# Optimization experiments

Measured on AMD Instinct MI355X. Metric: run time of the kernel, lower is better.

Reference implementation:

```python
import jax, jax.numpy as jnp
import numpy as np
import math

B, L, D, H = 2, 2048, 1024, 16
d = D // H

def setup_inputs() -> dict:
    key = jax.random.key(0)
    ks = jax.random.split(key, 12)
    s = 0.02
    return {
        "x": jax.random.normal(ks[0], (B, L, D), jnp.float32),
        "Wqkv_w": jax.random.normal(ks[1], (D, 3 * D), jnp.float32) * s,
        "Wqkv_b": jax.random.normal(ks[2], (3 * D,), jnp.float32) * s,
        "out_w": jax.random.normal(ks[3], (D, D), jnp.float32) * s,
        "out_b": jax.random.normal(ks[4], (D,), jnp.float32) * s,
        "W_static": jnp.zeros((H, d, d), jnp.float32),
        "Lambda_raw": jax.random.uniform(ks[5], (H, d, d), jnp.float32, -3.0, 3.0),
        "Gamma": jax.random.uniform(ks[6], (H, d, d), jnp.float32, -0.5 / math.sqrt(d), 0.5 / math.sqrt(d)),
        "gate_w1": jax.random.normal(ks[7], (D, D // 2), jnp.float32) * s,
        "gate_b1": jax.random.normal(ks[8], (D // 2,), jnp.float32) * s,
        "gate_w2": jax.random.normal(ks[9], (D // 2, H), jnp.float32) * s,
        "gate_b2": jax.random.normal(ks[10], (H,), jnp.float32) * s,
    }

def _forward(x, Wqkv_w, Wqkv_b, out_w, out_b, W_static, Lambda_raw, Gamma,
             gate_w1, gate_b1, gate_w2, gate_b2):
    scale = 1.0 / math.sqrt(d)
    qkv = x @ Wqkv_w + Wqkv_b                              # (B,L,3D)
    qkv = qkv.reshape(B, L, 3, H, d).transpose(2, 0, 3, 1, 4)  # (3,B,H,L,d)
    q, k, v = qkv[0], qkv[1], qkv[2]

    # --- causal softmax attention branch ---
    scores = jnp.einsum('bhid,bhjd->bhij', q, k) * scale
    mask = jnp.triu(jnp.full((L, L), -10000.0, scores.dtype), 1)
    attn = jax.nn.softmax(scores + mask, axis=-1)
    y_softmax = jnp.einsum('bhij,bhjd->bhid', attn, v)     # (B,H,L,d)

    # --- STP fast-weight branch: decaying Hebbian state recurrence ---
    k_stp = k * scale
    retention = 1.0 - jax.nn.sigmoid(Lambda_raw)           # (H,d,d)
    def step(state, qkv_t):
        q_t, k_t, v_t = qkv_t                              # each (B,H,d)
        hebbian = v_t[..., :, None] * k_t[..., None, :]    # (B,H,d,d)
        state = retention * state + Gamma * hebbian
        y_t = jnp.einsum('bhij,bhj->bhi', W_static + state, q_t)
        return state, y_t
    qkv_seq = (q.transpose(2, 0, 1, 3), k_stp.transpose(2, 0, 1, 3), v.transpose(2, 0, 1, 3))
    state0 = jnp.zeros((B, H, d, d), x.dtype)
    _, y_stp = jax.lax.scan(step, state0, qkv_seq)         # (L,B,H,d)
    y_stp = y_stp.transpose(1, 2, 0, 3)                    # (B,H,L,d)

    # --- learned gate ---
    h = jax.nn.gelu(x @ gate_w1 + gate_b1, approximate=False)
    alpha = jax.nn.sigmoid(h @ gate_w2 + gate_b2)          # (B,L,H)
    alpha = alpha.transpose(0, 2, 1)[..., None]            # (B,H,L,1)

    y = alpha * y_softmax + (1.0 - alpha) * y_stp          # (B,H,L,d)
    y = y.transpose(0, 2, 1, 3).reshape(B, L, D)
    return y @ out_w + out_b

def reference(x, Wqkv_w, Wqkv_b, out_w, out_b, W_static, Lambda_raw, Gamma,
              gate_w1, gate_b1, gate_w2, gate_b2):
    return _forward(x, Wqkv_w, Wqkv_b, out_w, out_b, W_static, Lambda_raw, Gamma,
                    gate_w1, gate_b1, gate_w2, gate_b2)
```

## Files before the change

### kernel.cpp

```cpp
#include <hip/hip_runtime.h>
#include <cstdint>
#include <cstddef>

#define B_ 2
#define L_ 2048
#define D_ 1024
#define H_ 16
#define DH 64

typedef __attribute__((ext_vector_type(8))) short bf16x8;
typedef __attribute__((ext_vector_type(4))) float f32x4;
typedef unsigned short u16;

__device__ inline u16 f2bf(float f) {
  unsigned u = __builtin_bit_cast(unsigned, f);
  u += 0x7fffu + ((u >> 16) & 1u);
  return (u16)(u >> 16);
}

__device__ inline float bf2f(u16 x) {
  return __builtin_bit_cast(float, (unsigned)x << 16);
}

template <int CTRL>
__device__ inline float dpp_mov(float x) {
  int t = __builtin_amdgcn_update_dpp(0, __builtin_bit_cast(int, x), CTRL, 0xf, 0xf, true);
  return __builtin_bit_cast(float, t);
}

#define GLDS16(ldst, gsrc)                                              \
  __builtin_amdgcn_global_load_lds(                                    \
      (const __attribute__((address_space(1))) void*)(gsrc),           \
      (__attribute__((address_space(3))) void*)(ldst), 16, 0, 0)

__device__ inline void stp_upd(float4& z, const float4 r, const float4 g,
                               const float4 wlc, float vv,
                               float kx, float ky, float kz, float kw) {
  z.x = fmaf(r.x, z.x, fmaf(g.x * vv, kx, wlc.x));
  z.y = fmaf(r.y, z.y, fmaf(g.y * vv, ky, wlc.y));
  z.z = fmaf(r.z, z.z, fmaf(g.z * vv, kz, wlc.z));
  z.w = fmaf(r.w, z.w, fmaf(g.w * vv, kw, wlc.w));
}

__device__ inline void stp_upd1(float4& z, const float4 r, const float4 g,
                                float vv, float kx, float ky, float kz, float kw) {
  z.x = fmaf(r.x, z.x, (g.x * vv) * kx);
  z.y = fmaf(r.y, z.y, (g.y * vv) * ky);
  z.z = fmaf(r.z, z.z, (g.z * vv) * kz);
  z.w = fmaf(r.w, z.w, (g.w * vv) * kw);
}

__device__ inline float stp_dot(const float4 z, float qx, float qy, float qz, float qw) {
  float p = z.x * qx;
  p = fmaf(z.y, qy, p);
  p = fmaf(z.z, qz, p);
  p = fmaf(z.w, qw, p);
  return p;
}

__device__ inline float dpp_red16(float p) {
  p = p + dpp_mov<0x128>(p);
  p = p + dpp_mov<0x124>(p);
  p = p + dpp_mov<0x122>(p);
  p = p + dpp_mov<0x121>(p);
  return p;
}


__device__ inline void d_transpose(const float* __restrict__ in,
                                   u16* __restrict__ out, int R, int C,
                                   int bx, int by, float tile[32][33], int tid) {
  const int tx = tid & 31, ty = tid >> 5;
  const int c0 = bx * 32, r0 = by * 32;
#pragma unroll
  for (int j = 0; j < 4; ++j)
    tile[ty + j * 8][tx] = in[(size_t)(r0 + ty + j * 8) * C + c0 + tx];
  __syncthreads();
#pragma unroll
  for (int j = 0; j < 4; ++j)
    out[(size_t)(c0 + ty + j * 8) * R + r0 + tx] = f2bf(tile[tx][ty + j * 8]);
}

__global__ __launch_bounds__(256) void prep_fused(
    const float* __restrict__ x, u16* __restrict__ xbf,
    const float* __restrict__ wqkv_w, u16* __restrict__ wqkvT,
    const float* __restrict__ out_w, u16* __restrict__ owT,
    const float* __restrict__ g_w1, u16* __restrict__ g1T,
    const float* __restrict__ lam, const float* __restrict__ gma,
    float* __restrict__ retb, float* __restrict__ gamb,
    float* __restrict__ retb64) {
  __shared__ float tile[32][33];
  const int bid = blockIdx.x, tid = threadIdx.x;
  if (bid < 4096) {
    int i = bid * 256 + tid;
    float4 v = ((const float4*)x)[i];
    ushort4 o;
    o.x = f2bf(v.x); o.y = f2bf(v.y); o.z = f2bf(v.z); o.w = f2bf(v.w);
    ((ushort4*)xbf)[i] = o;
  } else if (bid < 7168) {
    int r = bid - 4096;
    d_transpose(wqkv_w, wqkvT, 1024, 3072, r % 96, r / 96, tile, tid);
  } else if (bid < 8192) {
    int r = bid - 7168;
    d_transpose(out_w, owT, 1024, 1024, r % 32, r / 32, tile, tid);
  } else if (bid < 8704) {
    int r = bid - 8192;
    d_transpose(g_w1, g1T, 1024, 512, r % 16, r / 16, tile, tid);
  } else {
    int i = (bid - 8704) * 256 + tid;
    float l = lam[i];
    float r = 1.f / (1.f + expf(l));
    retb[i] = r;
    gamb[i] = gma[i] * 0.125f;
    float r2 = r * r;
    float r4 = r2 * r2;
    float r8 = r4 * r4;
    float r16 = r8 * r8;
    float r32 = r16 * r16;
    retb64[i] = r32 * r32;
  }
}


struct GemmP {
  const u16* A; const u16* Bt; int M, N, K;
  const float* bias;
  u16* qb; u16* kb; u16* vtb;
  float* hout;
  float* outp;
};

template <int EPI>
__device__ void gemm_body(const GemmP& p, int lin0, int nwgx, int nwgtot,
                          u16* As, u16* Bs, u16* tileT) {
  const int tid = threadIdx.x;
  const int lane = tid & 63;
  const int w = tid >> 6;
  const int wr = w >> 1, wc = w & 1;
  const int lr = lane & 15, lk = lane >> 4;
  const int cpx = nwgtot >> 3;
  const int lin = (lin0 & 7) * cpx + (lin0 >> 3);
  const int m0 = (lin / nwgx) * 128, n0 = (lin % nwgx) * 128;

  f32x4 acc[4][4];
#pragma unroll
  for (int i = 0; i < 4; ++i)
#pragma unroll
    for (int j = 0; j < 4; ++j) acc[i][j] = (f32x4){0.f, 0.f, 0.f, 0.f};

  for (int k0 = 0; k0 < p.K; k0 += 32) {
    __syncthreads();
#pragma unroll
    for (int it = 0; it < 2; ++it) {
      int idx = it * 256 + tid;
      int row = idx >> 2, ch = idx & 3;
      GLDS16(&As[idx * 8], p.A + (size_t)(m0 + row) * p.K + k0 + ch * 8);
      GLDS16(&Bs[idx * 8], p.Bt + (size_t)(n0 + row) * p.K + k0 + ch * 8);
    }
    __syncthreads();
    bf16x8 af[4], bfr[4];
#pragma unroll
    for (int mr = 0; mr < 4; ++mr)
      af[mr] = *(const bf16x8*)&As[(wr * 64 + mr * 16 + lr) * 32 + lk * 8];
#pragma unroll
    for (int nr = 0; nr < 4; ++nr)
      bfr[nr] = *(const bf16x8*)&Bs[(wc * 64 + nr * 16 + lr) * 32 + lk * 8];
#pragma unroll
    for (int mr = 0; mr < 4; ++mr)
#pragma unroll
      for (int nr = 0; nr < 4; ++nr)
        acc[mr][nr] = __builtin_amdgcn_mfma_f32_16x16x32_bf16(af[mr], bfr[nr], acc[mr][nr], 0, 0, 0);
  }

  if constexpr (EPI == 0) {
    if (n0 < 2048) {
#pragma unroll
      for (int mr = 0; mr < 4; ++mr)
#pragma unroll
        for (int nr = 0; nr < 4; ++nr) {
          const int col = n0 + wc * 64 + nr * 16 + lr;
#pragma unroll
          for (int rr = 0; rr < 4; ++rr) {
            const int row = m0 + wr * 64 + mr * 16 + lk * 4 + rr;
            float v = acc[mr][nr][rr] + p.bias[col];
            int which = col >> 10, hh = (col >> 6) & 15, ii = col & 63;
            int b = row >> 11, ll = row & 2047;
            size_t bi = ((size_t)(b * 16 + hh) * L_ + ll) * 64 + ii;
            if (which == 0) p.qb[bi] = f2bf(v * 0.125f);
            else            p.kb[bi] = f2bf(v);
          }
        }
    } else {
#pragma unroll
      for (int mr = 0; mr < 4; ++mr)
#pragma unroll
        for (int nr = 0; nr < 4; ++nr) {
          const int cl = wc * 64 + nr * 16 + lr;
          const float bv = p.bias[n0 + cl];
#pragma unroll
          for (int rr = 0; rr < 4; ++rr) {
            const int rl = wr * 64 + mr * 16 + lk * 4 + rr;
            tileT[cl * 136 + rl] = f2bf(acc[mr][nr][rr] + bv);
          }
        }
      __syncthreads();
      const int c = tid >> 1, h = tid & 1;
      const int vcol = (n0 - 2048) + c;
      const int hh = vcol >> 6, ii = vcol & 63;
      const int b = m0 >> 11;
      const int ll0 = (m0 & 2047) + h * 64;
      u16* dst = p.vtb + ((size_t)(b * 16 + hh) * 64 + ii) * L_ + ll0;
      const u16* src = &tileT[c * 136 + h * 64];
#pragma unroll
      for (int k = 0; k < 8; ++k)
        *(int4*)(dst + k * 8) = *(const int4*)(src + k * 8);
    }
  } else {
#pragma unroll
    for (int mr = 0; mr < 4; ++mr)
#pragma unroll
      for (int nr = 0; nr < 4; ++nr) {
        const int col = n0 + wc * 64 + nr * 16 + lr;
#pragma unroll
        for (int rr = 0; rr < 4; ++rr) {
          const int row = m0 + wr * 64 + mr * 16 + lk * 4 + rr;
          float v = acc[mr][nr][rr] + p.bias[col];
          if constexpr (EPI == 1) {
            float g = 0.5f * v * (1.f + erff(v * 0.70710678118f));
            p.hout[(size_t)row * p.N + col] = g;
          } else {
            p.outp[(size_t)row * p.N + col] = v;
          }
        }
      }
  }
}

__global__ __launch_bounds__(256, 2) void gemm01_kernel(GemmP p0, GemmP p1) {
  __shared__ u16 As[128 * 32];
  __shared__ u16 Bs[128 * 32];
  __shared__ u16 tileT[128 * 136];
  const int bid = blockIdx.x;
  if (bid < 768) gemm_body<0>(p0, bid, 24, 768, As, Bs, tileT);
  else           gemm_body<1>(p1, bid - 768, 4, 128, As, Bs, tileT);
}

__global__ __launch_bounds__(256, 2) void gemm2_kernel(GemmP p) {
  __shared__ u16 As[128 * 32];
  __shared__ u16 Bs[128 * 32];
  const int lin0 = (int)blockIdx.x + 8 * (int)blockIdx.y;
  gemm_body<2>(p, lin0, 8, 256, As, Bs, nullptr);
}


__global__ __launch_bounds__(256) void alpha_kernel(
    const float* __restrict__ hbuf, const float* __restrict__ w2,
    const float* __restrict__ b2, float* __restrict__ alp) {
  const int tid = threadIdx.x;
  const int row = blockIdx.x * 16 + (tid >> 4);
  const int n = tid & 15;
  const float4* h4 = (const float4*)(hbuf + (size_t)row * 512);
  float acc = 0.f;
#pragma unroll 2
  for (int kk = 0; kk < 128; ++kk) {
    float4 hv = h4[kk];
    acc = fmaf(hv.x, w2[(kk * 4 + 0) * 16 + n], acc);
    acc = fmaf(hv.y, w2[(kk * 4 + 1) * 16 + n], acc);
    acc = fmaf(hv.z, w2[(kk * 4 + 2) * 16 + n], acc);
    acc = fmaf(hv.w, w2[(kk * 4 + 3) * 16 + n], acc);
  }
  float z = acc + b2[n];
  alp[row * 16 + n] = 1.f / (1.f + __expf(-z));
}


__device__ void attn_body(int lin, u16* sbuf,
                          const u16* __restrict__ qb, const u16* __restrict__ kb,
                          const u16* __restrict__ vtb, float* __restrict__ ysm) {
  u16* Ks = sbuf;
  u16* Vts = sbuf + 4096;
  u16* Pl = sbuf + 8192;
  const int tid = threadIdx.x, lane = tid & 63, w = tid >> 6;
  const int lr = lane & 15, lk = lane >> 4;
  const int bh = lin & 31;
  const int xp = lin >> 5;
  const int qtA = 31 - xp, qtB = xp;

  const u16* kbase0 = kb + (size_t)bh * (L_ * 64);
  const u16* vbase0 = vtb + (size_t)bh * (64 * L_);

  const size_t qbaseA = ((size_t)bh * L_ + qtA * 64 + w * 16 + lr) * 64;
  const size_t qbaseB = ((size_t)bh * L_ + qtB * 64 + w * 16 + lr) * 64;
  bf16x8 qfrA[2], qfrB[2];
  qfrA[0] = *(const bf16x8*)(qb + qbaseA + lk * 8);
  qfrA[1] = *(const bf16x8*)(qb + qbaseA + 32 + lk * 8);
  qfrB[0] = *(const bf16x8*)(qb + qbaseB + lk * 8);
  qfrB[1] = *(const bf16x8*)(qb + qbaseB + 32 + lk * 8);

  f32x4 yaccA[4], yaccB[4];
  float mrowA[4], lrowA[4], mrowB[4], lrowB[4];
#pragma unroll
  for (int i = 0; i < 4; ++i) {
    yaccA[i] = (f32x4){0.f, 0.f, 0.f, 0.f};
    yaccB[i] = (f32x4){0.f, 0.f, 0.f, 0.f};
    mrowA[i] = -1e30f; mrowB[i] = -1e30f;
    lrowA[i] = 0.f;    lrowB[i] = 0.f;
  }

  auto process = [&](const bf16x8* qfr, f32x4* yacc, float* mrow, float* lrow,
                     bool maskTile) {
    f32x4 s[4];
#pragma unroll
    for (int f = 0; f < 4; ++f) {
      f32x4 sf = (f32x4){0.f, 0.f, 0.f, 0.f};
#pragma unroll
      for (int ss = 0; ss < 2; ++ss) {
        bf16x8 kfr = *(const bf16x8*)&Ks[(f * 16 + lr) * 64 +
                                         (((ss * 4 + lk) ^ (lr & 7)) * 8)];
        sf = __builtin_amdgcn_mfma_f32_16x16x32_bf16(qfr[ss], kfr, sf, 0, 0, 0);
      }
      s[f] = sf;
    }
    if (maskTile) {
#pragma unroll
      for (int f = 0; f < 4; ++f)
#pragma unroll
        for (int rr = 0; rr < 4; ++rr)
          if (f * 16 + lr > w * 16 + lk * 4 + rr) s[f][rr] = -1e30f;
    }
    float mx[4];
#pragma unroll
    for (int rr = 0; rr < 4; ++rr) {
      float m = fmaxf(fmaxf(s[0][rr], s[1][rr]), fmaxf(s[2][rr], s[3][rr]));
      m = fmaxf(m, dpp_mov<0x128>(m));
      m = fmaxf(m, dpp_mov<0x124>(m));
      m = fmaxf(m, dpp_mov<0x122>(m));
      m = fmaxf(m, dpp_mov<0x121>(m));
      mx[rr] = m;
    }
    bool need = (mx[0] > mrow[0] + 8.f) | (mx[1] > mrow[1] + 8.f) |
                (mx[2] > mrow[2] + 8.f) | (mx[3] > mrow[3] + 8.f);
    if (__any(need)) {
#pragma unroll
      for (int rr = 0; rr < 4; ++rr) {
        float mn = fmaxf(mrow[rr], mx[rr]);
        float c = __expf(mrow[rr] - mn);
        lrow[rr] *= c;
#pragma unroll
        for (int nf = 0; nf < 4; ++nf) yacc[nf][rr] *= c;
        mrow[rr] = mn;
      }
    }
    u16* pw = Pl + w * 1024;
#pragma unroll
    for (int rr = 0; rr < 4; ++rr) {
      const int prow = lk * 4 + rr;
      float rs = 0.f;
#pragma unroll
      for (int f = 0; f < 4; ++f) {
        float pv = __expf(s[f][rr] - mrow[rr]);
        rs += pv;
        int chunk = f * 2 + (lr >> 3);
        pw[prow * 64 + ((chunk ^ (prow & 7)) * 8) + (lr & 7)] = f2bf(pv);
      }
      rs = rs + dpp_mov<0x128>(rs);
      rs = rs + dpp_mov<0x124>(rs);
      rs = rs + dpp_mov<0x122>(rs);
      rs = rs + dpp_mov<0x121>(rs);
      lrow[rr] += rs;
    }
#pragma unroll
    for (int s2 = 0; s2 < 2; ++s2) {
      bf16x8 pa = *(const bf16x8*)&pw[lr * 64 + (((s2 * 4 + lk) ^ (lr & 7)) * 8)];
#pragma unroll
      for (int nf = 0; nf < 4; ++nf) {
        bf16x8 vfr = *(const bf16x8*)&Vts[(nf * 16 + lr) * 64 +
                                          (((s2 * 4 + lk) ^ (lr & 7)) * 8)];
        yacc[nf] = __builtin_amdgcn_mfma_f32_16x16x32_bf16(pa, vfr, yacc[nf], 0, 0, 0);
      }
    }
  };

  const int nkv = qtA + 1;
  for (int kt = 0; kt < nkv; ++kt) {
    const int kv0 = kt * 64;
    __syncthreads();
#pragma unroll
    for (int it = 0; it < 2; ++it) {
      int idx = it * 256 + tid;
      int row = idx >> 3, ch = idx & 7;
      int sch = (ch ^ (row & 7)) * 8;
      *(int4*)&Ks[row * 64 + sch] =
          *(const int4*)(kbase0 + (size_t)(kv0 + row) * 64 + ch * 8);
      *(int4*)&Vts[row * 64 + sch] =
          *(const int4*)(vbase0 + (size_t)row * L_ + kv0 + ch * 8);
    }
    __syncthreads();

    process(qfrA, yaccA, mrowA, lrowA, kt == qtA);
    if (kt <= qtB) process(qfrB, yaccB, mrowB, lrowB, kt == qtB);
  }

#pragma unroll
  for (int nf = 0; nf < 4; ++nf)
#pragma unroll
    for (int rr = 0; rr < 4; ++rr) {
      int rowl = w * 16 + lk * 4 + rr;
      int col = nf * 16 + lr;
      ysm[((size_t)bh * L_ + qtA * 64 + rowl) * 64 + col] = yaccA[nf][rr] / lrowA[rr];
      ysm[((size_t)bh * L_ + qtB * 64 + rowl) * 64 + col] = yaccB[nf][rr] / lrowB[rr];
    }
}


__device__ void stp1_body(int bid, u16* Klds,
                          const u16* __restrict__ kb, const u16* __restrict__ vtb,
                          const float* __restrict__ retb,
                          const float* __restrict__ gamb,
                          float* __restrict__ slocal) {
  const int tid = threadIdx.x, lane = tid & 63, w = tid >> 6;
  const int bh = bid >> 5, c = bid & 31;
  const int hh = bh & 15;
  const int m = lane >> 4, j4 = (lane & 15) * 4;
  const int i0m = w * 16 + m * 4;

  const u16* kcb = kb + ((size_t)bh * L_ + c * 64) * 64;
  GLDS16(&Klds[tid * 8], kcb + tid * 8);
  GLDS16(&Klds[2048 + tid * 8], kcb + 2048 + tid * 8);
  __syncthreads();

  const int hij = (hh * 64 + i0m) * 64 + j4;
  const float4 r0 = *(const float4*)(retb + hij);
  const float4 r1 = *(const float4*)(retb + hij + 64);
  const float4 r2 = *(const float4*)(retb + hij + 128);
  const float4 r3 = *(const float4*)(retb + hij + 192);
  const float4 g0 = *(const float4*)(gamb + hij);
  const float4 g1 = *(const float4*)(gamb + hij + 64);
  const float4 g2 = *(const float4*)(gamb + hij + 128);
  const float4 g3 = *(const float4*)(gamb + hij + 192);
  const u16* vbp = vtb + ((size_t)bh * 64 + i0m) * L_ + c * 64;

  float4 s0 = {0,0,0,0}, s1 = {0,0,0,0}, s2 = {0,0,0,0}, s3 = {0,0,0,0};
#pragma unroll 1
  for (int t8 = 0; t8 < 8; ++t8) {
    const bf16x8 va = *(const bf16x8*)(vbp + t8 * 8);
    const bf16x8 vb = *(const bf16x8*)(vbp + L_ + t8 * 8);
    const bf16x8 vc = *(const bf16x8*)(vbp + 2 * L_ + t8 * 8);
    const bf16x8 vd = *(const bf16x8*)(vbp + 3 * L_ + t8 * 8);
#pragma unroll
    for (int tt = 0; tt < 8; ++tt) {
      const ushort4 k4u = *(const ushort4*)&Klds[(t8 * 8 + tt) * 64 + j4];
      const float kx = bf2f(k4u.x), ky = bf2f(k4u.y),
                  kz = bf2f(k4u.z), kw = bf2f(k4u.w);
      stp_upd1(s0, r0, g0, bf2f((u16)va[tt]), kx, ky, kz, kw);
      stp_upd1(s1, r1, g1, bf2f((u16)vb[tt]), kx, ky, kz, kw);
      stp_upd1(s2, r2, g2, bf2f((u16)vc[tt]), kx, ky, kz, kw);
      stp_upd1(s3, r3, g3, bf2f((u16)vd[tt]), kx, ky, kz, kw);
    }
  }
  float* sb = slocal + (((size_t)(bh * 32 + c) * 64) + i0m) * 64 + j4;
  *(float4*)(sb)       = s0;
  *(float4*)(sb + 64)  = s1;
  *(float4*)(sb + 128) = s2;
  *(float4*)(sb + 192) = s3;
}

__global__ __launch_bounds__(256, 2) void attn_stp1_kernel(
    const u16* __restrict__ qb, const u16* __restrict__ kb,
    const u16* __restrict__ vtb, float* __restrict__ ysm,
    const float* __restrict__ retb, const float* __restrict__ gamb,
    float* __restrict__ slocal) {
  __shared__ u16 sbuf[12288];
  const int bid = blockIdx.x;
  if (bid < 512) attn_body(bid, sbuf, qb, kb, vtb, ysm);
  else           stp1_body(bid - 512, sbuf, kb, vtb, retb, gamb, slocal);
}

__global__ __launch_bounds__(256) void stp_scan(
    const float* __restrict__ retb64, float* __restrict__ slocal) {
  const int idx = blockIdx.x * 256 + threadIdx.x;
  const int j = idx & 63, i1 = (idx >> 6) & 63, bh = idx >> 12;
  const int hh = bh & 15;
  const float r64 = retb64[(hh * 64 + i1) * 64 + j];
  float carry = 0.f;
  for (int c = 0; c < 32; ++c) {
    const size_t off = ((((size_t)bh * 32 + c) * 64 + i1) * 64 + j);
    const float sl = slocal[off];
    slocal[off] = carry;
    carry = fmaf(r64, carry, sl);
  }
}

__global__ __launch_bounds__(256, 4) void stp_pass2(
    const u16* __restrict__ qb, const u16* __restrict__ kb,
    const u16* __restrict__ vtb, const float* __restrict__ retb,
    const float* __restrict__ gamb, const float* __restrict__ wst,
    const float* __restrict__ slocal, float* __restrict__ ystp) {
  __shared__ u16 KQ[8192];
  const int tid = threadIdx.x, lane = tid & 63, w = tid >> 6;
  const int bh = blockIdx.x >> 5, c = blockIdx.x & 31;
  const int hh = bh & 15;
  const int m = lane >> 4, jc = lane & 15, j4 = jc * 4;
  const int i0m = w * 16 + m * 4;

  const size_t cb = ((size_t)bh * L_ + c * 64) * 64;
  GLDS16(&KQ[tid * 8], kb + cb + tid * 8);
  GLDS16(&KQ[2048 + tid * 8], kb + cb + 2048 + tid * 8);
  GLDS16(&KQ[4096 + tid * 8], qb + cb + tid * 8);
  GLDS16(&KQ[6144 + tid * 8], qb + cb + 2048 + tid * 8);
  __syncthreads();

  const int hij = (hh * 64 + i0m) * 64 + j4;
  const float4 r0 = *(const float4*)(retb + hij);
  const float4 r1 = *(const float4*)(retb + hij + 64);
  const float4 r2 = *(const float4*)(retb + hij + 128);
  const float4 r3 = *(const float4*)(retb + hij + 192);
  const float4 g0 = *(const float4*)(gamb + hij);
  const float4 g1 = *(const float4*)(gamb + hij + 64);
  const float4 g2 = *(const float4*)(gamb + hij + 128);
  const float4 g3 = *(const float4*)(gamb + hij + 192);
  const float4 w0 = *(const float4*)(wst + hij);
  const float4 w1 = *(const float4*)(wst + hij + 64);
  const float4 w2 = *(const float4*)(wst + hij + 128);
  const float4 w3 = *(const float4*)(wst + hij + 192);

  const float* sb = slocal + (((size_t)(bh * 32 + c) * 64) + i0m) * 64 + j4;
  float4 z0 = *(const float4*)(sb);
  float4 z1 = *(const float4*)(sb + 64);
  float4 z2 = *(const float4*)(sb + 128);
  float4 z3 = *(const float4*)(sb + 192);

  float4 wlc0, wlc1, wlc2, wlc3;
  wlc0.x = w0.x * (1.f - r0.x); wlc0.y = w0.y * (1.f - r0.y);
  wlc0.z = w0.z * (1.f - r0.z); wlc0.w = w0.w * (1.f - r0.w);
  wlc1.x = w1.x * (1.f - r1.x); wlc1.y = w1.y * (1.f - r1.y);
  wlc1.z = w1.z * (1.f - r1.z); wlc1.w = w1.w * (1.f - r1.w);
  wlc2.x = w2.x * (1.f - r2.x); wlc2.y = w2.y * (1.f - r2.y);
  wlc2.z = w2.z * (1.f - r2.z); wlc2.w = w2.w * (1.f - r2.w);
  wlc3.x = w3.x * (1.f - r3.x); wlc3.y = w3.y * (1.f - r3.y);
  wlc3.z = w3.z * (1.f - r3.z); wlc3.w = w3.w * (1.f - r3.w);
  z0.x += w0.x; z0.y += w0.y; z0.z += w0.z; z0.w += w0.w;
  z1.x += w1.x; z1.y += w1.y; z1.z += w1.z; z1.w += w1.w;
  z2.x += w2.x; z2.y += w2.y; z2.z += w2.z; z2.w += w2.w;
  z3.x += w3.x; z3.y += w3.y; z3.z += w3.z; z3.w += w3.w;

  const u16* vbp = vtb + ((size_t)bh * 64 + i0m) * L_ + c * 64;
  float* yp = ystp + cb + i0m;

#pragma unroll 1
  for (int t8 = 0; t8 < 8; ++t8) {
    const bf16x8 va = *(const bf16x8*)(vbp + t8 * 8);
    const bf16x8 vb = *(const bf16x8*)(vbp + L_ + t8 * 8);
    const bf16x8 vc = *(const bf16x8*)(vbp + 2 * L_ + t8 * 8);
    const bf16x8 vd = *(const bf16x8*)(vbp + 3 * L_ + t8 * 8);
#pragma unroll
    for (int tt = 0; tt < 8; ++tt) {
      const int t = t8 * 8 + tt;
      const ushort4 k4u = *(const ushort4*)&KQ[t * 64 + j4];
      const ushort4 q4u = *(const ushort4*)&KQ[4096 + t * 64 + j4];
      const float kx = bf2f(k4u.x), ky = bf2f(k4u.y),
                  kz = bf2f(k4u.z), kw = bf2f(k4u.w);
      const float qx = bf2f(q4u.x), qy = bf2f(q4u.y),
                  qz = bf2f(q4u.z), qw = bf2f(q4u.w);
      stp_upd(z0, r0, g0, wlc0, bf2f((u16)va[tt]), kx, ky, kz, kw);
      stp_upd(z1, r1, g1, wlc1, bf2f((u16)vb[tt]), kx, ky, kz, kw);
      stp_upd(z2, r2, g2, wlc2, bf2f((u16)vc[tt]), kx, ky, kz, kw);
      stp_upd(z3, r3, g3, wlc3, bf2f((u16)vd[tt]), kx, ky, kz, kw);
      float p0 = dpp_red16(stp_dot(z0, qx, qy, qz, qw));
      float p1 = dpp_red16(stp_dot(z1, qx, qy, qz, qw));
      float p2 = dpp_red16(stp_dot(z2, qx, qy, qz, qw));
      float p3 = dpp_red16(stp_dot(z3, qx, qy, qz, qw));
      if (jc == 0) {
        float4 yo;
        yo.x = p0 * 8.f; yo.y = p1 * 8.f; yo.z = p2 * 8.f; yo.w = p3 * 8.f;
        *(float4*)(yp + t * 64) = yo;
      }
    }
  }
}


__global__ __launch_bounds__(256) void blend_kernel(
    const float* __restrict__ ysm, const float* __restrict__ ystp,
    const float* __restrict__ alp, u16* __restrict__ ycomb) {
  int idx = blockIdx.x * 256 + threadIdx.x;
  int m = idx >> 8;
  int n4 = (idx & 255) * 4;
  int hh = n4 >> 6, ii = n4 & 63;
  int b = m >> 11, ll = m & 2047;
  size_t bi = ((size_t)(b * 16 + hh) * L_ + ll) * 64 + ii;
  float a = alp[m * 16 + hh];
  float4 s = *(const float4*)(ysm + bi);
  float4 t = *(const float4*)(ystp + bi);
  ushort4 o;
  o.x = f2bf(a * s.x + (1.f - a) * t.x);
  o.y = f2bf(a * s.y + (1.f - a) * t.y);
  o.z = f2bf(a * s.z + (1.f - a) * t.z);
  o.w = f2bf(a * s.w + (1.f - a) * t.w);
  *(ushort4*)(ycomb + (size_t)m * 1024 + n4) = o;
}


extern "C" void kernel_launch(void* const* d_in, const int* in_sizes, int n_in,
                              void* d_out, int out_size, void* d_ws, size_t ws_size,
                              hipStream_t stream) {
  const float* x       = (const float*)d_in[0];
  const float* wqkv_w  = (const float*)d_in[1];
  const float* wqkv_b  = (const float*)d_in[2];
  const float* out_w   = (const float*)d_in[3];
  const float* out_b   = (const float*)d_in[4];
  const float* w_stat  = (const float*)d_in[5];
  const float* lam     = (const float*)d_in[6];
  const float* gma     = (const float*)d_in[7];
  const float* g_w1    = (const float*)d_in[8];
  const float* g_b1    = (const float*)d_in[9];
  const float* g_w2    = (const float*)d_in[10];
  const float* g_b2    = (const float*)d_in[11];

  char* ws = (char*)d_ws;
  size_t off = 0;
  auto nxt = [&](size_t b) { size_t r = off; off += (b + 255) & ~(size_t)255; return r; };
  u16*   xbf   = (u16*)(ws + nxt((size_t)4096 * 1024 * 2));
  u16*   wqkvT = (u16*)(ws + nxt((size_t)3072 * 1024 * 2));
  u16*   owT   = (u16*)(ws + nxt((size_t)1024 * 1024 * 2));
  u16*   g1T   = (u16*)(ws + nxt((size_t)512 * 1024 * 2));
  u16*   qb    = (u16*)(ws + nxt((size_t)4194304 * 2));
  u16*   kb    = (u16*)(ws + nxt((size_t)4194304 * 2));
  u16*   vtb   = (u16*)(ws + nxt((size_t)4194304 * 2));
  float* ysm   = (float*)(ws + nxt((size_t)4194304 * 4));
  float* ystp  = (float*)(ws + nxt((size_t)4194304 * 4));
  size_t hbuf_off = nxt((size_t)4096 * 512 * 4);
  float* hbuf  = (float*)(ws + hbuf_off);
  u16*   ycomb = (u16*)(ws + nxt((size_t)4096 * 1024 * 2));
  float* slocal = (float*)(ws + hbuf_off);
  float* alp   = (float*)(ws + nxt((size_t)4096 * 16 * 4));
  float* retb  = (float*)(ws + nxt((size_t)65536 * 4));
  float* gamb  = (float*)(ws + nxt((size_t)65536 * 4));
  float* retb64= (float*)(ws + nxt((size_t)65536 * 4));

  dim3 blk(256);
  prep_fused<<<8960, blk, 0, stream>>>(x, xbf, wqkv_w, wqkvT, out_w, owT,
                                       g_w1, g1T, lam, gma, retb, gamb, retb64);

  GemmP p0 = {xbf, wqkvT, 4096, 3072, 1024, wqkv_b,
              qb, kb, vtb, nullptr, nullptr};
  GemmP p1 = {xbf, g1T, 4096, 512, 1024, g_b1,
              nullptr, nullptr, nullptr, hbuf, nullptr};
  gemm01_kernel<<<896, blk, 0, stream>>>(p0, p1);

  alpha_kernel<<<256, blk, 0, stream>>>(hbuf, g_w2, g_b2, alp);

  attn_stp1_kernel<<<1536, blk, 0, stream>>>(qb, kb, vtb, ysm,
                                             retb, gamb, slocal);

  stp_scan<<<512, blk, 0, stream>>>(retb64, slocal);
  stp_pass2<<<1024, blk, 0, stream>>>(qb, kb, vtb, retb, gamb, w_stat,
                                      slocal, ystp);

  blend_kernel<<<4096, blk, 0, stream>>>(ysm, ystp, alp, ycomb);

  GemmP p2 = {ycomb, owT, 4096, 1024, 1024, out_b,
              nullptr, nullptr, nullptr, nullptr, (float*)d_out};
  gemm2_kernel<<<dim3(8, 32), blk, 0, stream>>>(p2);
}
```

Measured before the change: 252.8 us.

## Split fused attention/STP kernel; run paired query tiles on separate wave groups

The fused attention plus STP pass-1 kernel is split into two separate launches. Attention now uses 512-thread blocks in which two groups of four waves each handle one of the paired query tiles (one long, one short) at the same time instead of one after the other, sharing the K/V tiles staged in LDS. This raises per-block parallelism and lowers register pressure per wave. In exchange, the attention and STP work can no longer overlap within a single launch, there is an extra kernel launch, and the waves handling the shorter tile sit idle at barriers once their tile is done.

```diff
diff --git a/kernel.cpp b/kernel.cpp
--- a/kernel.cpp
+++ b/kernel.cpp
@@ -274,41 +274,40 @@
 }
 
 
-__device__ void attn_body(int lin, u16* sbuf,
-                          const u16* __restrict__ qb, const u16* __restrict__ kb,
-                          const u16* __restrict__ vtb, float* __restrict__ ysm) {
-  u16* Ks = sbuf;
-  u16* Vts = sbuf + 4096;
-  u16* Pl = sbuf + 8192;
+__global__ __launch_bounds__(512, 4) void attn_kernel(
+    const u16* __restrict__ qb, const u16* __restrict__ kb,
+    const u16* __restrict__ vtb, float* __restrict__ ysm) {
+  __shared__ u16 Ks[64 * 64];
+  __shared__ u16 Vts[64 * 64];
+  __shared__ u16 Pl[8][1024];
   const int tid = threadIdx.x, lane = tid & 63, w = tid >> 6;
+  const int wg = w >> 2;
+  const int wl = w & 3;
   const int lr = lane & 15, lk = lane >> 4;
+  const int lin = (int)blockIdx.x + 16 * (int)blockIdx.y;
   const int bh = lin & 31;
   const int xp = lin >> 5;
   const int qtA = 31 - xp, qtB = xp;
+  const int qt = wg ? qtB : qtA;
 
   const u16* kbase0 = kb + (size_t)bh * (L_ * 64);
   const u16* vbase0 = vtb + (size_t)bh * (64 * L_);
 
-  const size_t qbaseA = ((size_t)bh * L_ + qtA * 64 + w * 16 + lr) * 64;
-  const size_t qbaseB = ((size_t)bh * L_ + qtB * 64 + w * 16 + lr) * 64;
-  bf16x8 qfrA[2], qfrB[2];
-  qfrA[0] = *(const bf16x8*)(qb + qbaseA + lk * 8);
-  qfrA[1] = *(const bf16x8*)(qb + qbaseA + 32 + lk * 8);
-  qfrB[0] = *(const bf16x8*)(qb + qbaseB + lk * 8);
-  qfrB[1] = *(const bf16x8*)(qb + qbaseB + 32 + lk * 8);
-
-  f32x4 yaccA[4], yaccB[4];
-  float mrowA[4], lrowA[4], mrowB[4], lrowB[4];
+  const size_t qbase = ((size_t)bh * L_ + qt * 64 + wl * 16 + lr) * 64;
+  bf16x8 qfr[2];
+  qfr[0] = *(const bf16x8*)(qb + qbase + lk * 8);
+  qfr[1] = *(const bf16x8*)(qb + qbase + 32 + lk * 8);
+
+  f32x4 yacc[4];
+  float mrow[4], lrow[4];
 #pragma unroll
   for (int i = 0; i < 4; ++i) {
-    yaccA[i] = (f32x4){0.f, 0.f, 0.f, 0.f};
-    yaccB[i] = (f32x4){0.f, 0.f, 0.f, 0.f};
-    mrowA[i] = -1e30f; mrowB[i] = -1e30f;
-    lrowA[i] = 0.f;    lrowB[i] = 0.f;
-  }
-
-  auto process = [&](const bf16x8* qfr, f32x4* yacc, float* mrow, float* lrow,
-                     bool maskTile) {
+    yacc[i] = (f32x4){0.f, 0.f, 0.f, 0.f};
+    mrow[i] = -1e30f;
+    lrow[i] = 0.f;
+  }
+
+  auto process = [&](bool maskTile) {
     f32x4 s[4];
 #pragma unroll
     for (int f = 0; f < 4; ++f) {
@@ -326,7 +325,7 @@
       for (int f = 0; f < 4; ++f)
 #pragma unroll
         for (int rr = 0; rr < 4; ++rr)
-          if (f * 16 + lr > w * 16 + lk * 4 + rr) s[f][rr] = -1e30f;
+          if (f * 16 + lr > wl * 16 + lk * 4 + rr) s[f][rr] = -1e30f;
     }
     float mx[4];
 #pragma unroll
@@ -351,7 +350,7 @@
         mrow[rr] = mn;
       }
     }
-    u16* pw = Pl + w * 1024;
+    u16* pw = &Pl[w][0];
 #pragma unroll
     for (int rr = 0; rr < 4; ++rr) {
       const int prow = lk * 4 + rr;
@@ -385,10 +384,8 @@
   for (int kt = 0; kt < nkv; ++kt) {
     const int kv0 = kt * 64;
     __syncthreads();
-#pragma unroll
-    for (int it = 0; it < 2; ++it) {
-      int idx = it * 256 + tid;
-      int row = idx >> 3, ch = idx & 7;
+    {
+      int row = tid >> 3, ch = tid & 7;
       int sch = (ch ^ (row & 7)) * 8;
       *(int4*)&Ks[row * 64 + sch] =
           *(const int4*)(kbase0 + (size_t)(kv0 + row) * 64 + ch * 8);
@@ -397,29 +394,28 @@
     }
     __syncthreads();
 
-    process(qfrA, yaccA, mrowA, lrowA, kt == qtA);
-    if (kt <= qtB) process(qfrB, yaccB, mrowB, lrowB, kt == qtB);
+    if (wg == 0)            process(kt == qtA);
+    else if (kt <= qtB)     process(kt == qtB);
   }
 
 #pragma unroll
   for (int nf = 0; nf < 4; ++nf)
 #pragma unroll
     for (int rr = 0; rr < 4; ++rr) {
-      int rowl = w * 16 + lk * 4 + rr;
+      int rowl = wl * 16 + lk * 4 + rr;
       int col = nf * 16 + lr;
-      ysm[((size_t)bh * L_ + qtA * 64 + rowl) * 64 + col] = yaccA[nf][rr] / lrowA[rr];
-      ysm[((size_t)bh * L_ + qtB * 64 + rowl) * 64 + col] = yaccB[nf][rr] / lrowB[rr];
-    }
-}
-
-
-__device__ void stp1_body(int bid, u16* Klds,
-                          const u16* __restrict__ kb, const u16* __restrict__ vtb,
-                          const float* __restrict__ retb,
-                          const float* __restrict__ gamb,
-                          float* __restrict__ slocal) {
+      ysm[((size_t)bh * L_ + qt * 64 + rowl) * 64 + col] = yacc[nf][rr] / lrow[rr];
+    }
+}
+
+
+__global__ __launch_bounds__(256, 4) void stp_pass1(
+    const u16* __restrict__ kb, const u16* __restrict__ vtb,
+    const float* __restrict__ retb, const float* __restrict__ gamb,
+    float* __restrict__ slocal) {
+  __shared__ u16 Klds[4096];
   const int tid = threadIdx.x, lane = tid & 63, w = tid >> 6;
-  const int bh = bid >> 5, c = bid & 31;
+  const int bh = blockIdx.x >> 5, c = blockIdx.x & 31;
   const int hh = bh & 15;
   const int m = lane >> 4, j4 = (lane & 15) * 4;
   const int i0m = w * 16 + m * 4;
@@ -463,17 +459,6 @@
   *(float4*)(sb + 64)  = s1;
   *(float4*)(sb + 128) = s2;
   *(float4*)(sb + 192) = s3;
-}
-
-__global__ __launch_bounds__(256, 2) void attn_stp1_kernel(
-    const u16* __restrict__ qb, const u16* __restrict__ kb,
-    const u16* __restrict__ vtb, float* __restrict__ ysm,
-    const float* __restrict__ retb, const float* __restrict__ gamb,
-    float* __restrict__ slocal) {
-  __shared__ u16 sbuf[12288];
-  const int bid = blockIdx.x;
-  if (bid < 512) attn_body(bid, sbuf, qb, kb, vtb, ysm);
-  else           stp1_body(bid - 512, sbuf, kb, vtb, retb, gamb, slocal);
 }
 
 __global__ __launch_bounds__(256) void stp_scan(
@@ -650,9 +635,9 @@
 
   alpha_kernel<<<256, blk, 0, stream>>>(hbuf, g_w2, g_b2, alp);
 
-  attn_stp1_kernel<<<1536, blk, 0, stream>>>(qb, kb, vtb, ysm,
-                                             retb, gamb, slocal);
-
+  attn_kernel<<<dim3(16, 32), dim3(512), 0, stream>>>(qb, kb, vtb, ysm);
+
+  stp_pass1<<<1024, blk, 0, stream>>>(kb, vtb, retb, gamb, slocal);
   stp_scan<<<512, blk, 0, stream>>>(retb64, slocal);
   stp_pass2<<<1024, blk, 0, stream>>>(qb, kb, vtb, retb, gamb, w_stat,
                                       slocal, ystp);
```

New measurement: 263.0 us. +4.0%, slower.
